# Kernel tuning notes

Measured on AMD Instinct MI355X. Metric: run time of the kernel, lower is better.

## Reference

```python
import jax, jax.numpy as jnp
import numpy as np

N_NODES = 50000
N_EDGES = 500000
HIDDEN = 128
OUT = 64


def _sage_conv(x, edge_index, Wl, Wr, b):
    # PyG SAGEConv (aggr='mean', root_weight=True):
    # out_i = Wl @ mean_{j->i} x_j + Wr @ x_i + b
    src, dst = edge_index[0], edge_index[1]
    msgs = x[src]                                         # [E, d] gather
    summed = jax.ops.segment_sum(msgs, dst, num_segments=N_NODES)   # [N, d]
    deg = jax.ops.segment_sum(jnp.ones((msgs.shape[0],), x.dtype), dst,
                              num_segments=N_NODES)       # [N]
    agg = summed / jnp.maximum(deg, 1.0)[:, None]         # mean (0 if no in-edges)
    return agg @ Wl + x @ Wr + b


def setup_inputs() -> dict:
    key = jax.random.key(0)
    ks = jax.random.split(key, 11)
    s = 1.0 / np.sqrt(HIDDEN)
    inp = {
        "x": jax.random.normal(ks[0], (N_NODES, HIDDEN), jnp.float32),
        "edge_index": jax.random.randint(ks[1], (2, N_EDGES), 0, N_NODES, jnp.int32),
        "W1l": jax.random.normal(ks[2], (HIDDEN, HIDDEN), jnp.float32) * s,
        "W1r": jax.random.normal(ks[3], (HIDDEN, HIDDEN), jnp.float32) * s,
        "b1": jax.random.normal(ks[4], (HIDDEN,), jnp.float32) * s,
        "W2l": jax.random.normal(ks[5], (HIDDEN, HIDDEN), jnp.float32) * s,
        "W2r": jax.random.normal(ks[6], (HIDDEN, HIDDEN), jnp.float32) * s,
        "b2": jax.random.normal(ks[7], (HIDDEN,), jnp.float32) * s,
        "W3l": jax.random.normal(ks[8], (HIDDEN, OUT), jnp.float32) * s,
        "W3r": jax.random.normal(ks[9], (HIDDEN, OUT), jnp.float32) * s,
        "b3": jax.random.normal(ks[10], (OUT,), jnp.float32) * s,
    }
    return inp


def reference(x, edge_index, W1l, W1r, b1, W2l, W2r, b2, W3l, W3r, b3):
    h = jax.nn.relu(_sage_conv(x, edge_index, W1l, W1r, b1))
    h = jax.nn.relu(_sage_conv(h, edge_index, W2l, W2r, b2))
    return _sage_conv(h, edge_index, W3l, W3r, b3)
```

## Files before the change

kernel.cpp:

```cpp
#include <hip/hip_runtime.h>

typedef unsigned int u32;
typedef unsigned short u16;
typedef __bf16 bf16x8 __attribute__((ext_vector_type(8)));
typedef float f32x4 __attribute__((ext_vector_type(4)));

#define HID 128
#define MAXD 64

__device__ __forceinline__ u16 f2bf(float f) {
  u32 u = __float_as_uint(f);
  u32 r = u + 0x7FFFu + ((u >> 16) & 1u);
  return (u16)(r >> 16);
}
__device__ __forceinline__ float bflo(u32 a) { return __uint_as_float(a << 16); }
__device__ __forceinline__ float bfhi(u32 a) { return __uint_as_float(a & 0xFFFF0000u); }

__device__ __forceinline__ void pack_one(const float* __restrict__ W,
                                         u16* __restrict__ P, int N, int t) {
  int lane = t & 63;
  int kt = (t >> 6) & 3;
  int nt = t >> 8;
  int colc = nt * 16 + (lane & 15);
  int krow = kt * 32 + (lane >> 4) * 8;
  u16* d = P + (size_t)t * 8;
#pragma unroll
  for (int j = 0; j < 8; ++j) d[j] = f2bf(W[(krow + j) * N + colc]);
}

__global__ void k_scat(const int* __restrict__ src, const int* __restrict__ dst,
                       int* __restrict__ deg, int* __restrict__ col, int E,
                       const float* __restrict__ x, u32* __restrict__ xb, int n4,
                       const float* __restrict__ W1l, const float* __restrict__ W1r,
                       const float* __restrict__ W2l, const float* __restrict__ W2r,
                       const float* __restrict__ W3l, const float* __restrict__ W3r,
                       u16* __restrict__ P1l, u16* __restrict__ P1r,
                       u16* __restrict__ P2l, u16* __restrict__ P2r,
                       u16* __restrict__ P3l, u16* __restrict__ P3r) {
  int t = blockIdx.x * blockDim.x + threadIdx.x;
  int e2 = t * 2;
  if (e2 + 1 < E) {
    int2 s = *(const int2*)(src + e2);
    int2 d = *(const int2*)(dst + e2);
    int r0 = atomicAdd(&deg[d.x], 1);
    if (r0 < MAXD) col[(d.x << 6) + r0] = s.x;
    int r1 = atomicAdd(&deg[d.y], 1);
    if (r1 < MAXD) col[(d.y << 6) + r1] = s.y;
  } else if (e2 < E) {
    int d = dst[e2];
    int r = atomicAdd(&deg[d], 1);
    if (r < MAXD) col[(d << 6) + r] = src[e2];
  }
  if (t < 10240) {
    if (t < 2048) pack_one(W1l, P1l, 128, t);
    else if (t < 4096) pack_one(W1r, P1r, 128, t - 2048);
    else if (t < 6144) pack_one(W2l, P2l, 128, t - 4096);
    else if (t < 8192) pack_one(W2r, P2r, 128, t - 6144);
    else if (t < 9216) pack_one(W3l, P3l, 64, t - 8192);
    else pack_one(W3r, P3r, 64, t - 9216);
    return;
  }
  int c = t - 10240;
  if (c < n4) {
    f32x4 v = ((const f32x4*)x)[c];
    xb[c * 2] = (u32)f2bf(v[0]) | ((u32)f2bf(v[1]) << 16);
    xb[c * 2 + 1] = (u32)f2bf(v[2]) | ((u32)f2bf(v[3]) << 16);
  }
}

__global__ void k_agg(const u16* __restrict__ feat, const int* __restrict__ deg,
                      const int* __restrict__ col, u16* __restrict__ agg, int n) {
  int w = (blockIdx.x * blockDim.x + threadIdx.x) >> 6;
  int lane = threadIdx.x & 63;
  if (w >= n) return;
  int slot = col[(w << 6) | lane];
  int dtru = deg[w];
  int dcap = min(dtru, MAXD);
  int g = lane >> 4;
  int sub = lane & 15;
  const uint4* fb = (const uint4*)feat;
  float a0 = 0.f, a1 = 0.f, a2 = 0.f, a3 = 0.f;
  float a4 = 0.f, a5 = 0.f, a6 = 0.f, a7 = 0.f;
  for (int k = 0; k < dcap; k += 8) {
    int e0 = k + g;
    int e1 = k + 4 + g;
    bool p0 = e0 < dcap;
    bool p1 = e1 < dcap;
    int j0 = __shfl(slot, e0 & 63);
    int j1 = __shfl(slot, e1 & 63);
    uint4 x0 = fb[(size_t)(p0 ? j0 : 0) * 16 + sub];
    uint4 x1 = fb[(size_t)(p1 ? j1 : 0) * 16 + sub];
    if (!p0) x0.x = x0.y = x0.z = x0.w = 0u;
    if (!p1) x1.x = x1.y = x1.z = x1.w = 0u;
    a0 += bflo(x0.x); a1 += bfhi(x0.x); a2 += bflo(x0.y); a3 += bfhi(x0.y);
    a4 += bflo(x0.z); a5 += bfhi(x0.z); a6 += bflo(x0.w); a7 += bfhi(x0.w);
    a0 += bflo(x1.x); a1 += bfhi(x1.x); a2 += bflo(x1.y); a3 += bfhi(x1.y);
    a4 += bflo(x1.z); a5 += bfhi(x1.z); a6 += bflo(x1.w); a7 += bfhi(x1.w);
  }
  a0 += __shfl_xor(a0, 16); a0 += __shfl_xor(a0, 32);
  a1 += __shfl_xor(a1, 16); a1 += __shfl_xor(a1, 32);
  a2 += __shfl_xor(a2, 16); a2 += __shfl_xor(a2, 32);
  a3 += __shfl_xor(a3, 16); a3 += __shfl_xor(a3, 32);
  a4 += __shfl_xor(a4, 16); a4 += __shfl_xor(a4, 32);
  a5 += __shfl_xor(a5, 16); a5 += __shfl_xor(a5, 32);
  a6 += __shfl_xor(a6, 16); a6 += __shfl_xor(a6, 32);
  a7 += __shfl_xor(a7, 16); a7 += __shfl_xor(a7, 32);
  if (g == 0) {
    float inv = 1.0f / (float)max(dtru, 1);
    uint4 o;
    o.x = (u32)f2bf(a0 * inv) | ((u32)f2bf(a1 * inv) << 16);
    o.y = (u32)f2bf(a2 * inv) | ((u32)f2bf(a3 * inv) << 16);
    o.z = (u32)f2bf(a4 * inv) | ((u32)f2bf(a5 * inv) << 16);
    o.w = (u32)f2bf(a6 * inv) | ((u32)f2bf(a7 * inv) << 16);
    *((uint4*)(agg + (size_t)w * HID) + sub) = o;
  }
}

template <int NT, int MR, bool RELU, bool OUTF32>
__global__ void k_gemm(const u16* __restrict__ Aagg, const u16* __restrict__ Ah,
                       const u16* __restrict__ Pl, const u16* __restrict__ Pr,
                       const float* __restrict__ bias, void* __restrict__ outp,
                       int mtiles, int n) {
  int wv = (blockIdx.x * blockDim.x + threadIdx.x) >> 6;
  int lane = threadIdx.x & 63;
  int tile0 = wv * MR;
  if (tile0 >= mtiles) return;

  f32x4 acc[MR][NT];
#pragma unroll
  for (int mr = 0; mr < MR; ++mr)
#pragma unroll
    for (int nt = 0; nt < NT; ++nt) acc[mr][nt] = 0.f;

  int rl = lane & 15;
  int kg = lane >> 4;
  int tm[MR];
  const u16 *pa[MR], *ph[MR];
#pragma unroll
  for (int mr = 0; mr < MR; ++mr) {
    tm[mr] = min(tile0 + mr, mtiles - 1);
    int row = tm[mr] * 16 + rl;
    pa[mr] = Aagg + (size_t)row * HID + kg * 8;
    ph[mr] = Ah + (size_t)row * HID + kg * 8;
  }

#pragma unroll
  for (int kt = 0; kt < 4; ++kt) {
    bf16x8 af[MR];
#pragma unroll
    for (int mr = 0; mr < MR; ++mr) af[mr] = *(const bf16x8*)(pa[mr] + kt * 32);
#pragma unroll
    for (int nt = 0; nt < NT; ++nt) {
      bf16x8 bf = *(const bf16x8*)(Pl + ((size_t)(nt * 4 + kt) * 64 + lane) * 8);
#pragma unroll
      for (int mr = 0; mr < MR; ++mr)
        acc[mr][nt] = __builtin_amdgcn_mfma_f32_16x16x32_bf16(af[mr], bf, acc[mr][nt], 0, 0, 0);
    }
  }
#pragma unroll
  for (int kt = 0; kt < 4; ++kt) {
    bf16x8 af[MR];
#pragma unroll
    for (int mr = 0; mr < MR; ++mr) af[mr] = *(const bf16x8*)(ph[mr] + kt * 32);
#pragma unroll
    for (int nt = 0; nt < NT; ++nt) {
      bf16x8 bf = *(const bf16x8*)(Pr + ((size_t)(nt * 4 + kt) * 64 + lane) * 8);
#pragma unroll
      for (int mr = 0; mr < MR; ++mr)
        acc[mr][nt] = __builtin_amdgcn_mfma_f32_16x16x32_bf16(af[mr], bf, acc[mr][nt], 0, 0, 0);
    }
  }

  const int N = NT * 16;
  int rq = lane >> 4;
#pragma unroll
  for (int mr = 0; mr < MR; ++mr) {
#pragma unroll
    for (int nt = 0; nt < NT; ++nt) {
      float bv = bias[nt * 16 + rl];
#pragma unroll
      for (int j = 0; j < 4; ++j) {
        float v = acc[mr][nt][j] + bv;
        if (RELU) v = fmaxf(v, 0.f);
        int r = tm[mr] * 16 + rq * 4 + j;
        if (OUTF32)
          ((float*)outp)[(size_t)r * N + nt * 16 + rl] = v;
        else
          ((u16*)outp)[(size_t)r * N + nt * 16 + rl] = f2bf(v);
      }
    }
  }
}

extern "C" void kernel_launch(void* const* d_in, const int* in_sizes, int n_in,
                              void* d_out, int out_size, void* d_ws, size_t ws_size,
                              hipStream_t stream) {
  const float* x = (const float*)d_in[0];
  const int* ei = (const int*)d_in[1];
  const float* W1l = (const float*)d_in[2];
  const float* W1r = (const float*)d_in[3];
  const float* b1 = (const float*)d_in[4];
  const float* W2l = (const float*)d_in[5];
  const float* W2r = (const float*)d_in[6];
  const float* b2 = (const float*)d_in[7];
  const float* W3l = (const float*)d_in[8];
  const float* W3r = (const float*)d_in[9];
  const float* b3 = (const float*)d_in[10];

  const int E = in_sizes[1] / 2;
  const int N = in_sizes[0] / HID;
  const int* esrc = ei;
  const int* edst = ei + E;

  char* wp = (char*)d_ws;
  auto alloc = [&](size_t b) {
    char* p = wp;
    wp += (b + 255) & ~(size_t)255;
    return p;
  };
  int* deg = (int*)alloc((size_t)N * 4);
  int* col = (int*)alloc((size_t)N * MAXD * 4);
  u16* featA = (u16*)alloc((size_t)N * HID * 2);
  u16* featB = (u16*)alloc((size_t)N * HID * 2);
  u16* aggb = (u16*)alloc((size_t)N * HID * 2);
  u16* P1l = (u16*)alloc(8 * 4 * 64 * 8 * 2);
  u16* P1r = (u16*)alloc(8 * 4 * 64 * 8 * 2);
  u16* P2l = (u16*)alloc(8 * 4 * 64 * 8 * 2);
  u16* P2r = (u16*)alloc(8 * 4 * 64 * 8 * 2);
  u16* P3l = (u16*)alloc(4 * 4 * 64 * 8 * 2);
  u16* P3r = (u16*)alloc(4 * 4 * 64 * 8 * 2);

  hipMemsetAsync(deg, 0, (size_t)N * 4, stream);

  int n4 = N * (HID / 4);
  int spn = 10240 + n4;
  int ehalf = (E + 1) / 2;
  if (ehalf > spn) spn = ehalf;
  k_scat<<<(spn + 255) / 256, 256, 0, stream>>>(
      esrc, edst, deg, col, E, x, (u32*)featA, n4,
      W1l, W1r, W2l, W2r, W3l, W3r, P1l, P1r, P2l, P2r, P3l, P3r);

  int ab = (N * 64 + 255) / 256;
  int mtiles = N / 16;
  int gwaves = (mtiles + 1) / 2;
  int gb = (gwaves * 64 + 255) / 256;

  k_agg<<<ab, 256, 0, stream>>>(featA, deg, col, aggb, N);
  k_gemm<8, 2, true, false><<<gb, 256, 0, stream>>>(aggb, featA, P1l, P1r, b1, featB, mtiles, N);
  k_agg<<<ab, 256, 0, stream>>>(featB, deg, col, aggb, N);
  k_gemm<8, 2, true, false><<<gb, 256, 0, stream>>>(aggb, featB, P2l, P2r, b2, featA, mtiles, N);
  k_agg<<<ab, 256, 0, stream>>>(featA, deg, col, aggb, N);
  k_gemm<4, 2, false, true><<<gb, 256, 0, stream>>>(aggb, featA, P3l, P3r, b3, (float*)d_out, mtiles, N);
}
```

Before: 236.4 us.

## Split neighbor aggregation into column quarters and store adjacency as 16-bit

The mean-aggregation kernel now launches four waves per node, one per 32-column quarter. Each lane gathers one 32-bit word per neighbor instead of a 16-byte vector, giving more waves in flight to hide gather latency and using fewer registers per wave. The adjacency slot array is stored as u16 instead of int, which halves its footprint and read traffic. In exchange, each node's slot list and degree are read four times, gathers become 64-byte segments, and node indices must stay below 65536.

```diff
diff --git a/kernel.cpp b/kernel.cpp
--- a/kernel.cpp
+++ b/kernel.cpp
@@ -29,7 +29,7 @@
 }
 
 __global__ void k_scat(const int* __restrict__ src, const int* __restrict__ dst,
-                       int* __restrict__ deg, int* __restrict__ col, int E,
+                       int* __restrict__ deg, u16* __restrict__ col, int E,
                        const float* __restrict__ x, u32* __restrict__ xb, int n4,
                        const float* __restrict__ W1l, const float* __restrict__ W1r,
                        const float* __restrict__ W2l, const float* __restrict__ W2r,
@@ -43,13 +43,13 @@
     int2 s = *(const int2*)(src + e2);
     int2 d = *(const int2*)(dst + e2);
     int r0 = atomicAdd(&deg[d.x], 1);
-    if (r0 < MAXD) col[(d.x << 6) + r0] = s.x;
+    if (r0 < MAXD) col[(d.x << 6) + r0] = (u16)s.x;
     int r1 = atomicAdd(&deg[d.y], 1);
-    if (r1 < MAXD) col[(d.y << 6) + r1] = s.y;
+    if (r1 < MAXD) col[(d.y << 6) + r1] = (u16)s.y;
   } else if (e2 < E) {
     int d = dst[e2];
     int r = atomicAdd(&deg[d], 1);
-    if (r < MAXD) col[(d << 6) + r] = src[e2];
+    if (r < MAXD) col[(d << 6) + r] = (u16)src[e2];
   }
   if (t < 10240) {
     if (t < 2048) pack_one(W1l, P1l, 128, t);
@@ -69,18 +69,19 @@
 }
 
 __global__ void k_agg(const u16* __restrict__ feat, const int* __restrict__ deg,
-                      const int* __restrict__ col, u16* __restrict__ agg, int n) {
-  int w = (blockIdx.x * blockDim.x + threadIdx.x) >> 6;
+                      const u16* __restrict__ col, u16* __restrict__ agg, int n) {
+  int unit = (blockIdx.x * blockDim.x + threadIdx.x) >> 6;
   int lane = threadIdx.x & 63;
-  if (w >= n) return;
+  int q = unit / n;
+  int w = unit - q * n;
+  if (q >= 4) return;
   int slot = col[(w << 6) | lane];
   int dtru = deg[w];
   int dcap = min(dtru, MAXD);
   int g = lane >> 4;
   int sub = lane & 15;
-  const uint4* fb = (const uint4*)feat;
-  float a0 = 0.f, a1 = 0.f, a2 = 0.f, a3 = 0.f;
-  float a4 = 0.f, a5 = 0.f, a6 = 0.f, a7 = 0.f;
+  const u32* fb = (const u32*)feat + q * 16 + sub;
+  float a0 = 0.f, a1 = 0.f, b0 = 0.f, b1 = 0.f;
   for (int k = 0; k < dcap; k += 8) {
     int e0 = k + g;
     int e1 = k + 4 + g;
@@ -88,31 +89,21 @@
     bool p1 = e1 < dcap;
     int j0 = __shfl(slot, e0 & 63);
     int j1 = __shfl(slot, e1 & 63);
-    uint4 x0 = fb[(size_t)(p0 ? j0 : 0) * 16 + sub];
-    uint4 x1 = fb[(size_t)(p1 ? j1 : 0) * 16 + sub];
-    if (!p0) x0.x = x0.y = x0.z = x0.w = 0u;
-    if (!p1) x1.x = x1.y = x1.z = x1.w = 0u;
-    a0 += bflo(x0.x); a1 += bfhi(x0.x); a2 += bflo(x0.y); a3 += bfhi(x0.y);
-    a4 += bflo(x0.z); a5 += bfhi(x0.z); a6 += bflo(x0.w); a7 += bfhi(x0.w);
-    a0 += bflo(x1.x); a1 += bfhi(x1.x); a2 += bflo(x1.y); a3 += bfhi(x1.y);
-    a4 += bflo(x1.z); a5 += bfhi(x1.z); a6 += bflo(x1.w); a7 += bfhi(x1.w);
-  }
+    u32 x0 = fb[(size_t)(p0 ? j0 : 0) * 64];
+    u32 x1 = fb[(size_t)(p1 ? j1 : 0) * 64];
+    if (!p0) x0 = 0u;
+    if (!p1) x1 = 0u;
+    a0 += bflo(x0); a1 += bfhi(x0);
+    b0 += bflo(x1); b1 += bfhi(x1);
+  }
+  a0 += b0;
+  a1 += b1;
   a0 += __shfl_xor(a0, 16); a0 += __shfl_xor(a0, 32);
   a1 += __shfl_xor(a1, 16); a1 += __shfl_xor(a1, 32);
-  a2 += __shfl_xor(a2, 16); a2 += __shfl_xor(a2, 32);
-  a3 += __shfl_xor(a3, 16); a3 += __shfl_xor(a3, 32);
-  a4 += __shfl_xor(a4, 16); a4 += __shfl_xor(a4, 32);
-  a5 += __shfl_xor(a5, 16); a5 += __shfl_xor(a5, 32);
-  a6 += __shfl_xor(a6, 16); a6 += __shfl_xor(a6, 32);
-  a7 += __shfl_xor(a7, 16); a7 += __shfl_xor(a7, 32);
   if (g == 0) {
     float inv = 1.0f / (float)max(dtru, 1);
-    uint4 o;
-    o.x = (u32)f2bf(a0 * inv) | ((u32)f2bf(a1 * inv) << 16);
-    o.y = (u32)f2bf(a2 * inv) | ((u32)f2bf(a3 * inv) << 16);
-    o.z = (u32)f2bf(a4 * inv) | ((u32)f2bf(a5 * inv) << 16);
-    o.w = (u32)f2bf(a6 * inv) | ((u32)f2bf(a7 * inv) << 16);
-    *((uint4*)(agg + (size_t)w * HID) + sub) = o;
+    ((u32*)agg)[(size_t)w * 64 + q * 16 + sub] =
+        (u32)f2bf(a0 * inv) | ((u32)f2bf(a1 * inv) << 16);
   }
 }
 
@@ -219,7 +210,7 @@
     return p;
   };
   int* deg = (int*)alloc((size_t)N * 4);
-  int* col = (int*)alloc((size_t)N * MAXD * 4);
+  u16* col = (u16*)alloc((size_t)N * MAXD * 2);
   u16* featA = (u16*)alloc((size_t)N * HID * 2);
   u16* featB = (u16*)alloc((size_t)N * HID * 2);
   u16* aggb = (u16*)alloc((size_t)N * HID * 2);
@@ -240,7 +231,7 @@
       esrc, edst, deg, col, E, x, (u32*)featA, n4,
       W1l, W1r, W2l, W2r, W3l, W3r, P1l, P1r, P2l, P2r, P3l, P3r);
 
-  int ab = (N * 64 + 255) / 256;
+  int ab = ((size_t)4 * N * 64 + 255) / 256;
   int mtiles = N / 16;
   int gwaves = (mtiles + 1) / 2;
   int gb = (gwaves * 64 + 255) / 256;
```

New measurement: 334.3 us. 41.4% more time.
